# Kernel tuning notes

Hardware: AMD Instinct MI355X
Metric: run time of the kernel (lower is better)

## Reference

```python
import jax, jax.numpy as jnp
import numpy as np

N = 12000       # num nodes
E = 384000      # num edges (avg degree 32)
F_IN = 512      # num_feats
H = 64          # gnn_hid_dim (== anchor_dim)
C = 7           # num_cls
SIGMA = 1.0


def setup_inputs() -> dict:
    key = jax.random.key(0)
    ks = jax.random.split(key, 9)
    scale = lambda fan_in: 1.0 / np.sqrt(fan_in)
    return {
        "x": jax.random.normal(ks[0], (N, F_IN), dtype=jnp.float32),
        "W1": jax.random.normal(ks[1], (F_IN, H), dtype=jnp.float32) * scale(F_IN),
        "b1": jnp.zeros((H,), dtype=jnp.float32),
        "W2": jax.random.normal(ks[2], (H, H), dtype=jnp.float32) * scale(H),
        "b2": jnp.zeros((H,), dtype=jnp.float32),
        "aux": jax.random.normal(ks[3], (H,), dtype=jnp.float32),
        "clf_W": jax.random.normal(ks[4], (2 * H, C), dtype=jnp.float32) * scale(2 * H),
        "clf_b": jnp.zeros((C,), dtype=jnp.float32),
        "edge_index": jax.random.randint(ks[5], (2, E), 0, N, dtype=jnp.int64),
    }


def gcn_conv(x, W, b, src, dst, n):
    # GCNConv: D^{-1/2} (A + I) D^{-1/2} X W + b, with self-loops
    h = x @ W                                                   # [N, out]
    deg = jax.ops.segment_sum(jnp.ones(src.shape[0], h.dtype), dst,
                              num_segments=n) + 1.0             # +1 for self-loop
    inv_sqrt = jax.lax.rsqrt(deg)
    norm = inv_sqrt[src] * inv_sqrt[dst]                        # [E]
    agg = jax.ops.segment_sum(h[src] * norm[:, None], dst, num_segments=n)
    agg = agg + h / deg[:, None]                                # self-loop term (norm = 1/deg)
    return agg + b


def reference(x, W1, b1, W2, b2, aux, clf_W, clf_b, edge_index):
    src, dst = edge_index[0], edge_index[1]
    n = x.shape[0]
    h = jax.nn.relu(gcn_conv(x, W1, b1, src, dst, n))
    h = gcn_conv(h, W2, b2, src, dst, n)                        # [N, H]
    # kernel aggregate: pairwise Gaussian kernel on cosine scores
    a = aux / jnp.maximum(jnp.linalg.norm(aux), 1e-12)          # F.normalize
    hn = jnp.maximum(jnp.linalg.norm(h, axis=-1), 1e-8)         # cosine_similarity eps
    score = (h @ a) / hn                                        # [N]
    diff = score[None, :] - score[:, None]                      # [N, N]
    kappa = jnp.exp(-(diff * diff) / (SIGMA * SIGMA))           # [N, N]
    z = (kappa @ h) / jnp.sum(kappa, axis=1, keepdims=True)     # [N, H]
    return jnp.concatenate([h, z], axis=-1) @ clf_W + clf_b     # [N, C]
```

## Files before the change

### kernel.cpp

```cpp
#include <hip/hip_runtime.h>
#include <hip/hip_bf16.h>
#include <hip/hip_fp16.h>

#define N_NODES 12000
#define N_EDGES 384000
#define F_IN 512
#define H 64
#define C_CLS 7
#define KTERMS 16
#define PAD 96
#define CSTR 32
#define MOM_BLKS 768
#define MSTR 1040
#define NB 4
#define GEMM_BLKS 188
#define FILL_BLKS 324

typedef __attribute__((ext_vector_type(8))) short bf16x8;
typedef __attribute__((ext_vector_type(4))) float f32x4;

__device__ __forceinline__ float wred_f(float x) {
    #pragma unroll
    for (int o = 32; o > 0; o >>= 1) x += __shfl_xor(x, o);
    return x;
}

__global__ __launch_bounds__(256) void init_k(const float* __restrict__ W1,
                                              unsigned short* __restrict__ w1Th,
                                              unsigned short* __restrict__ w1Tl,
                                              int* __restrict__ cur,
                                              double* __restrict__ M8) {
    int i = blockIdx.x * 256 + threadIdx.x;
    if (i < 64 * 512) {
        int n = i >> 9, k = i & 511;
        float v = W1[k * 64 + n];
        unsigned xb = __float_as_uint(v);
        float hf = __uint_as_float(xb & 0xffff0000u);
        w1Th[i] = (unsigned short)(xb >> 16);
        w1Tl[i] = (unsigned short)(__float_as_uint(v - hf) >> 16);
    }
    if (i < N_NODES) cur[i * CSTR] = 0;
    if (i < 8 * MSTR) M8[i] = 0.0;
}

__global__ __launch_bounds__(256) void k1_gemm_fill(const float* __restrict__ x,
                                                    const unsigned short* __restrict__ w1Th,
                                                    const unsigned short* __restrict__ w1Tl,
                                                    const int* __restrict__ ei,
                                                    __half* __restrict__ hbufH,
                                                    int* __restrict__ cur,
                                                    int* __restrict__ csrc) {
    const int b = blockIdx.x, t = threadIdx.x;
    if (b < GEMM_BLKS) {
        __shared__ unsigned short wh[64 * 72];
        __shared__ unsigned short wl[64 * 72];
        const int l = t & 63, w = t >> 6;
        const int lm = l & 15, lk = l >> 4;
        const int i0 = b * 64;
        const int arow = min(i0 + w * 16 + lm, N_NODES - 1);
        const float* xrow = x + (size_t)arow * F_IN;
        f32x4 acc[4];
        #pragma unroll
        for (int c = 0; c < 4; ++c) acc[c] = (f32x4){0.f, 0.f, 0.f, 0.f};
        for (int kc = 0; kc < 8; ++kc) {
            #pragma unroll
            for (int q = 0; q < 2; ++q) {
                int idx = t + q * 256;
                int n = idx >> 3, kg = idx & 7;
                *(uint4*)(&wh[n * 72 + kg * 8]) =
                    *(const uint4*)(w1Th + n * 512 + kc * 64 + kg * 8);
                *(uint4*)(&wl[n * 72 + kg * 8]) =
                    *(const uint4*)(w1Tl + n * 512 + kc * 64 + kg * 8);
            }
            __syncthreads();
            #pragma unroll
            for (int ks = 0; ks < 2; ++ks) {
                float4 v0 = *(const float4*)(xrow + kc * 64 + ks * 32 + lk * 8);
                float4 v1 = *(const float4*)(xrow + kc * 64 + ks * 32 + lk * 8 + 4);
                float xv[8] = {v0.x, v0.y, v0.z, v0.w, v1.x, v1.y, v1.z, v1.w};
                bf16x8 ah, al;
                #pragma unroll
                for (int j = 0; j < 8; ++j) {
                    unsigned xb = __float_as_uint(xv[j]);
                    float hf = __uint_as_float(xb & 0xffff0000u);
                    ah[j] = (short)(xb >> 16);
                    al[j] = (short)(__float_as_uint(xv[j] - hf) >> 16);
                }
                #pragma unroll
                for (int c = 0; c < 4; ++c) {
                    bf16x8 bh = *(const bf16x8*)(&wh[(c * 16 + lm) * 72 + ks * 32 + lk * 8]);
                    bf16x8 bl = *(const bf16x8*)(&wl[(c * 16 + lm) * 72 + ks * 32 + lk * 8]);
                    acc[c] = __builtin_amdgcn_mfma_f32_16x16x32_bf16(ah, bh, acc[c], 0, 0, 0);
                    acc[c] = __builtin_amdgcn_mfma_f32_16x16x32_bf16(ah, bl, acc[c], 0, 0, 0);
                    acc[c] = __builtin_amdgcn_mfma_f32_16x16x32_bf16(al, bh, acc[c], 0, 0, 0);
                }
            }
            __syncthreads();
        }
        #pragma unroll
        for (int c = 0; c < 4; ++c) {
            #pragma unroll
            for (int r = 0; r < 4; ++r) {
                int row = i0 + w * 16 + lk * 4 + r;
                if (row < N_NODES)
                    hbufH[(size_t)row * H + c * 16 + lm] = __float2half(acc[c][r]);
            }
        }
    } else {
        for (int e = (b - GEMM_BLKS) * 256 + t; e < N_EDGES; e += FILL_BLKS * 256) {
            int s = ei[e];
            int d = ei[N_EDGES + e];
            int pos = atomicAdd(&cur[d * CSTR], 1);
            if (pos < PAD) csrc[d * PAD + pos] = s;
        }
    }
}

__global__ __launch_bounds__(256) void agg1_k(const __half* __restrict__ hbufH,
                                              const float* __restrict__ b1,
                                              const int* __restrict__ cur,
                                              const int* __restrict__ csrc,
                                              __half* __restrict__ h1H) {
    __shared__ int2 sPair[NB * PAD];
    __shared__ int sDeg[NB];
    __shared__ float sIsd[NB];
    const int t = threadIdx.x, f = t & 63, w = t >> 6;
    const int base = blockIdx.x * NB;
    if (t < NB) {
        int d = cur[(base + t) * CSTR];
        sDeg[t] = min(d, PAD);
        sIsd[t] = rsqrtf((float)d + 1.f);
    }
    __syncthreads();
    for (int idx = t; idx < NB * PAD; idx += 256) {
        int n = idx / PAD, e = idx - n * PAD;
        if (e < sDeg[n]) {
            int s = csrc[(base + n) * PAD + e];
            sPair[idx] = make_int2(s, __float_as_int(rsqrtf((float)cur[s * CSTR] + 1.f)));
        }
    }
    __syncthreads();
    const int i = base + w;
    const int deg = sDeg[w];
    const float isd = sIsd[w];
    const int2* pp = sPair + w * PAD;
    float acc = 0.f;
    int e = 0;
    for (; e + 16 <= deg; e += 16) {
        float part = 0.f;
        #pragma unroll
        for (int u = 0; u < 16; ++u) {
            int2 p = pp[e + u];
            part += __half2float(hbufH[p.x * H + f]) * __int_as_float(p.y);
        }
        acc += part;
    }
    for (; e + 4 <= deg; e += 4) {
        int2 p0 = pp[e], p1 = pp[e+1], p2 = pp[e+2], p3 = pp[e+3];
        acc += __half2float(hbufH[p0.x * H + f]) * __int_as_float(p0.y)
             + __half2float(hbufH[p1.x * H + f]) * __int_as_float(p1.y)
             + __half2float(hbufH[p2.x * H + f]) * __int_as_float(p2.y)
             + __half2float(hbufH[p3.x * H + f]) * __int_as_float(p3.y);
    }
    for (; e < deg; ++e) {
        int2 p = pp[e];
        acc += __half2float(hbufH[p.x * H + f]) * __int_as_float(p.y);
    }
    float res = (acc + __half2float(hbufH[i * H + f]) * isd) * isd + b1[f];
    h1H[i * H + f] = __float2half(fmaxf(res, 0.f));
}

__global__ __launch_bounds__(256) void agg2_k(const __half* __restrict__ h1H,
                                              const float* __restrict__ W2,
                                              const float* __restrict__ b2,
                                              const float* __restrict__ aux,
                                              const int* __restrict__ cur,
                                              const int* __restrict__ csrc,
                                              __half* __restrict__ h2H,
                                              float* __restrict__ score) {
    __shared__ float w2s[64 * 64];
    __shared__ int2 sPair[NB * PAD];
    __shared__ int sDeg[NB];
    __shared__ float sIsd[NB];
    __shared__ float anorm[64];
    __shared__ float gsh[NB * 64];
    const int t = threadIdx.x, f = t & 63, w = t >> 6;
    const int base = blockIdx.x * NB;
    #pragma unroll
    for (int q = 0; q < 4; ++q) {
        int idx = t + q * 256;
        int r = idx >> 4, c4 = idx & 15;
        *(float4*)(&w2s[r * 64 + c4 * 4]) = *(const float4*)(W2 + r * H + c4 * 4);
    }
    if (t < NB) {
        int d = cur[(base + t) * CSTR];
        sDeg[t] = min(d, PAD);
        sIsd[t] = rsqrtf((float)d + 1.f);
    }
    if (t < 64) {
        float av = aux[t];
        anorm[t] = av * rsqrtf(fmaxf(wred_f(av * av), 1e-24f));
    }
    __syncthreads();
    for (int idx = t; idx < NB * PAD; idx += 256) {
        int n = idx / PAD, e = idx - n * PAD;
        if (e < sDeg[n]) {
            int s = csrc[(base + n) * PAD + e];
            sPair[idx] = make_int2(s, __float_as_int(rsqrtf((float)cur[s * CSTR] + 1.f)));
        }
    }
    __syncthreads();
    const int i = base + w;
    const int deg = sDeg[w];
    const float isd = sIsd[w];
    const int2* pp = sPair + w * PAD;
    float acc = 0.f;
    int e = 0;
    for (; e + 16 <= deg; e += 16) {
        float part = 0.f;
        #pragma unroll
        for (int u = 0; u < 16; ++u) {
            int2 p = pp[e + u];
            part += __half2float(h1H[p.x * H + f]) * __int_as_float(p.y);
        }
        acc += part;
    }
    for (; e + 4 <= deg; e += 4) {
        int2 p0 = pp[e], p1 = pp[e+1], p2 = pp[e+2], p3 = pp[e+3];
        acc += __half2float(h1H[p0.x * H + f]) * __int_as_float(p0.y)
             + __half2float(h1H[p1.x * H + f]) * __int_as_float(p1.y)
             + __half2float(h1H[p2.x * H + f]) * __int_as_float(p2.y)
             + __half2float(h1H[p3.x * H + f]) * __int_as_float(p3.y);
    }
    for (; e < deg; ++e) {
        int2 p = pp[e];
        acc += __half2float(h1H[p.x * H + f]) * __int_as_float(p.y);
    }
    float g = (acc + __half2float(h1H[i * H + f]) * isd) * isd;
    gsh[w * 64 + f] = g;
    __builtin_amdgcn_wave_barrier();
    float hv = b2[f];
    #pragma unroll 16
    for (int k = 0; k < 64; ++k) hv += gsh[w * 64 + k] * w2s[k * 64 + f];
    h2H[i * H + f] = __float2half(hv);
    float dp = wred_f(hv * anorm[f]);
    float nn = wred_f(hv * hv);
    if (f == 0) score[i] = dp / fmaxf(sqrtf(nn), 1e-8f);
}

__global__ __launch_bounds__(256) void momden_k(const __half* __restrict__ h2H,
                                                const float* __restrict__ score,
                                                double* __restrict__ M8) {
    const int t = threadIdx.x, f = t & 63, g = t >> 6;
    float accM[KTERMS], accD[KTERMS];
    #pragma unroll
    for (int k = 0; k < KTERMS; ++k) { accM[k] = 0.f; accD[k] = 0.f; }
    for (int j = blockIdx.x * 4 + g; j < N_NODES; j += MOM_BLKS * 4) {
        float sj = score[j];
        float wj = expf(-sj * sj);
        float hv = __half2float(h2H[j * H + f]);
        float tm = wj * hv, td = wj;
        #pragma unroll
        for (int k = 0; k < KTERMS; ++k) {
            accM[k] += tm; tm *= sj;
            accD[k] += td; td *= sj;
        }
    }
    __shared__ float Msh[4 * KTERMS * 64];
    __shared__ float Dsh[4 * KTERMS];
    #pragma unroll
    for (int k = 0; k < KTERMS; ++k) Msh[(g * KTERMS + k) * 64 + f] = accM[k];
    if (f == 0) {
        #pragma unroll
        for (int k = 0; k < KTERMS; ++k) Dsh[g * KTERMS + k] = accD[k];
    }
    __syncthreads();
    double* Mc = M8 + (size_t)(blockIdx.x & 7) * MSTR;
    for (int idx = t; idx < KTERMS * 64; idx += 256) {
        int k = idx >> 6, ff = idx & 63;
        float sum = Msh[(0 * KTERMS + k) * 64 + ff] + Msh[(1 * KTERMS + k) * 64 + ff]
                  + Msh[(2 * KTERMS + k) * 64 + ff] + Msh[(3 * KTERMS + k) * 64 + ff];
        unsafeAtomicAdd(&Mc[idx], (double)sum);
    }
    if (t < KTERMS) {
        float sum = Dsh[t] + Dsh[KTERMS + t] + Dsh[2 * KTERMS + t] + Dsh[3 * KTERMS + t];
        unsafeAtomicAdd(&Mc[1024 + t], (double)sum);
    }
}

__global__ __launch_bounds__(256) void final_k(const __half* __restrict__ h2H,
                                               const float* __restrict__ score,
                                               const double* __restrict__ M8,
                                               const float* __restrict__ clfW,
                                               const float* __restrict__ clfb,
                                               float* __restrict__ out) {
    __shared__ float Ms[KTERMS * 64];
    __shared__ float m0s[KTERMS];
    __shared__ float cw[128 * C_CLS];
    __shared__ float cb[8];
    __shared__ float zh[4 * 128];
    const int t = threadIdx.x, f = t & 63, w = t >> 6;
    for (int idx = t; idx < KTERMS * 64; idx += 256) {
        double s = 0.0;
        #pragma unroll
        for (int c = 0; c < 8; ++c) s += M8[(size_t)c * MSTR + idx];
        Ms[idx] = (float)s;
    }
    if (t < KTERMS) {
        double s = 0.0;
        #pragma unroll
        for (int c = 0; c < 8; ++c) s += M8[(size_t)c * MSTR + 1024 + t];
        m0s[t] = (float)s;
    }
    for (int idx = t; idx < 128 * C_CLS; idx += 256) cw[idx] = clfW[idx];
    if (t < C_CLS) cb[t] = clfb[t];
    __syncthreads();
    const int base = blockIdx.x * 16;
    for (int q = 0; q < 4; ++q) {
        int i = base + q * 4 + w;
        float s = score[i];
        float c = expf(-s * s);
        float t2 = 2.f * s;
        float num = 0.f, den = 0.f;
        #pragma unroll
        for (int k = 0; k < KTERMS; ++k) {
            num += c * Ms[k * 64 + f];
            den += c * m0s[k];
            c *= t2 * (1.0f / (float)(k + 1));
        }
        zh[w * 128 + f] = __half2float(h2H[i * H + f]);
        zh[w * 128 + 64 + f] = num / den;
        __builtin_amdgcn_wave_barrier();
        if (f < C_CLS) {
            float o = cb[f];
            #pragma unroll 8
            for (int u = 0; u < 128; ++u) o += zh[w * 128 + u] * cw[u * C_CLS + f];
            out[(size_t)i * C_CLS + f] = o;
        }
        __builtin_amdgcn_wave_barrier();
    }
}

extern "C" void kernel_launch(void* const* d_in, const int* in_sizes, int n_in,
                              void* d_out, int out_size, void* d_ws, size_t ws_size,
                              hipStream_t stream) {
    (void)in_sizes; (void)n_in; (void)out_size; (void)ws_size;
    const float* x    = (const float*)d_in[0];
    const float* W1   = (const float*)d_in[1];
    const float* b1   = (const float*)d_in[2];
    const float* W2   = (const float*)d_in[3];
    const float* b2   = (const float*)d_in[4];
    const float* aux  = (const float*)d_in[5];
    const float* clfW = (const float*)d_in[6];
    const float* clfb = (const float*)d_in[7];
    const int*   ei   = (const int*)d_in[8];
    float* out = (float*)d_out;
    char* ws = (char*)d_ws;

    __half* hbufH = (__half*)(ws + 0);
    __half* h1H   = (__half*)(ws + 1536000);
    __half* h2H   = (__half*)(ws + 3072000);
    float*  score = (float*)(ws + 4608000);
    int*    csrc  = (int*)  (ws + 4656000);
    int*    cur   = (int*)  (ws + 9264000);
    double* M8    = (double*)(ws + 10800000);
    unsigned short* w1Th = (unsigned short*)(ws + 10866560);
    unsigned short* w1Tl = (unsigned short*)(ws + 10932096);

    init_k<<<128, 256, 0, stream>>>(W1, w1Th, w1Tl, cur, M8);
    k1_gemm_fill<<<GEMM_BLKS + FILL_BLKS, 256, 0, stream>>>(x, w1Th, w1Tl, ei,
                                                            hbufH, cur, csrc);
    agg1_k<<<N_NODES / NB, 256, 0, stream>>>(hbufH, b1, cur, csrc, h1H);
    agg2_k<<<N_NODES / NB, 256, 0, stream>>>(h1H, W2, b2, aux, cur, csrc, h2H, score);
    momden_k<<<MOM_BLKS, 256, 0, stream>>>(h2H, score, M8);
    final_k<<<750, 256, 0, stream>>>(h2H, score, M8, clfW, clfb, out);
}
```

Measured before the change: 87.24 us.

## Double-buffer W1 tiles in GEMM and reuse edge pairs across aggregation kernels

The first-layer GEMM now double-buffers the W1 hi/lo tiles in shared memory and prefetches the next x chunk into registers, so global loads overlap the MFMA work and one barrier per iteration is removed. agg1 also writes its (source, normalization) pairs to a workspace buffer. agg2 then copies these pairs with vector loads instead of re-gathering csrc and the scattered degree counts. This costs double the LDS in the GEMM blocks and an extra global write in agg1. The agg2 copy reads full padded slots, some of which hold garbage past each node's degree, but those entries are never used.

Measured after the change: 89.30 us. 1.02x slower.

```diff
diff --git a/kernel.cpp b/kernel.cpp
--- a/kernel.cpp
+++ b/kernel.cpp
@@ -52,8 +52,8 @@
                                                     int* __restrict__ csrc) {
     const int b = blockIdx.x, t = threadIdx.x;
     if (b < GEMM_BLKS) {
-        __shared__ unsigned short wh[64 * 72];
-        __shared__ unsigned short wl[64 * 72];
+        __shared__ unsigned short wh[2][64 * 72];
+        __shared__ unsigned short wl[2][64 * 72];
         const int l = t & 63, w = t >> 6;
         const int lm = l & 15, lk = l >> 4;
         const int i0 = b * 64;
@@ -62,22 +62,47 @@
         f32x4 acc[4];
         #pragma unroll
         for (int c = 0; c < 4; ++c) acc[c] = (f32x4){0.f, 0.f, 0.f, 0.f};
+
+        #define STAGE_W(KC, BUF)                                                   \
+            do {                                                                   \
+                _Pragma("unroll")                                                  \
+                for (int q = 0; q < 2; ++q) {                                      \
+                    int idx = t + q * 256;                                         \
+                    int n = idx >> 3, kg = idx & 7;                                \
+                    *(uint4*)(&wh[BUF][n * 72 + kg * 8]) =                         \
+                        *(const uint4*)(w1Th + n * 512 + (KC) * 64 + kg * 8);      \
+                    *(uint4*)(&wl[BUF][n * 72 + kg * 8]) =                         \
+                        *(const uint4*)(w1Tl + n * 512 + (KC) * 64 + kg * 8);      \
+                }                                                                  \
+            } while (0)
+
+        float4 a0 = *(const float4*)(xrow + lk * 8);
+        float4 a1 = *(const float4*)(xrow + lk * 8 + 4);
+        float4 g0 = *(const float4*)(xrow + 32 + lk * 8);
+        float4 g1 = *(const float4*)(xrow + 32 + lk * 8 + 4);
+        STAGE_W(0, 0);
+        __syncthreads();
         for (int kc = 0; kc < 8; ++kc) {
-            #pragma unroll
-            for (int q = 0; q < 2; ++q) {
-                int idx = t + q * 256;
-                int n = idx >> 3, kg = idx & 7;
-                *(uint4*)(&wh[n * 72 + kg * 8]) =
-                    *(const uint4*)(w1Th + n * 512 + kc * 64 + kg * 8);
-                *(uint4*)(&wl[n * 72 + kg * 8]) =
-                    *(const uint4*)(w1Tl + n * 512 + kc * 64 + kg * 8);
+            const int cb = kc & 1;
+            float4 ca0 = a0, ca1 = a1, cg0 = g0, cg1 = g1;
+            if (kc < 7) {
+                const float* nx = xrow + (kc + 1) * 64;
+                a0 = *(const float4*)(nx + lk * 8);
+                a1 = *(const float4*)(nx + lk * 8 + 4);
+                g0 = *(const float4*)(nx + 32 + lk * 8);
+                g1 = *(const float4*)(nx + 32 + lk * 8 + 4);
+                STAGE_W(kc + 1, cb ^ 1);
             }
-            __syncthreads();
             #pragma unroll
             for (int ks = 0; ks < 2; ++ks) {
-                float4 v0 = *(const float4*)(xrow + kc * 64 + ks * 32 + lk * 8);
-                float4 v1 = *(const float4*)(xrow + kc * 64 + ks * 32 + lk * 8 + 4);
-                float xv[8] = {v0.x, v0.y, v0.z, v0.w, v1.x, v1.y, v1.z, v1.w};
+                float xv[8];
+                if (ks == 0) {
+                    xv[0]=ca0.x; xv[1]=ca0.y; xv[2]=ca0.z; xv[3]=ca0.w;
+                    xv[4]=ca1.x; xv[5]=ca1.y; xv[6]=ca1.z; xv[7]=ca1.w;
+                } else {
+                    xv[0]=cg0.x; xv[1]=cg0.y; xv[2]=cg0.z; xv[3]=cg0.w;
+                    xv[4]=cg1.x; xv[5]=cg1.y; xv[6]=cg1.z; xv[7]=cg1.w;
+                }
                 bf16x8 ah, al;
                 #pragma unroll
                 for (int j = 0; j < 8; ++j) {
@@ -88,8 +113,8 @@
                 }
                 #pragma unroll
                 for (int c = 0; c < 4; ++c) {
-                    bf16x8 bh = *(const bf16x8*)(&wh[(c * 16 + lm) * 72 + ks * 32 + lk * 8]);
-                    bf16x8 bl = *(const bf16x8*)(&wl[(c * 16 + lm) * 72 + ks * 32 + lk * 8]);
+                    bf16x8 bh = *(const bf16x8*)(&wh[cb][(c * 16 + lm) * 72 + ks * 32 + lk * 8]);
+                    bf16x8 bl = *(const bf16x8*)(&wl[cb][(c * 16 + lm) * 72 + ks * 32 + lk * 8]);
                     acc[c] = __builtin_amdgcn_mfma_f32_16x16x32_bf16(ah, bh, acc[c], 0, 0, 0);
                     acc[c] = __builtin_amdgcn_mfma_f32_16x16x32_bf16(ah, bl, acc[c], 0, 0, 0);
                     acc[c] = __builtin_amdgcn_mfma_f32_16x16x32_bf16(al, bh, acc[c], 0, 0, 0);
@@ -97,6 +122,7 @@
             }
             __syncthreads();
         }
+        #undef STAGE_W
         #pragma unroll
         for (int c = 0; c < 4; ++c) {
             #pragma unroll
@@ -120,7 +146,8 @@
                                               const float* __restrict__ b1,
                                               const int* __restrict__ cur,
                                               const int* __restrict__ csrc,
-                                              __half* __restrict__ h1H) {
+                                              __half* __restrict__ h1H,
+                                              int2* __restrict__ pairs) {
     __shared__ int2 sPair[NB * PAD];
     __shared__ int sDeg[NB];
     __shared__ float sIsd[NB];
@@ -136,7 +163,9 @@
         int n = idx / PAD, e = idx - n * PAD;
         if (e < sDeg[n]) {
             int s = csrc[(base + n) * PAD + e];
-            sPair[idx] = make_int2(s, __float_as_int(rsqrtf((float)cur[s * CSTR] + 1.f)));
+            int2 v = make_int2(s, __float_as_int(rsqrtf((float)cur[s * CSTR] + 1.f)));
+            sPair[idx] = v;
+            pairs[base * PAD + idx] = v;
         }
     }
     __syncthreads();
@@ -175,7 +204,7 @@
                                               const float* __restrict__ b2,
                                               const float* __restrict__ aux,
                                               const int* __restrict__ cur,
-                                              const int* __restrict__ csrc,
+                                              const int2* __restrict__ pairs,
                                               __half* __restrict__ h2H,
                                               float* __restrict__ score) {
     __shared__ float w2s[64 * 64];
@@ -201,13 +230,10 @@
         float av = aux[t];
         anorm[t] = av * rsqrtf(fmaxf(wred_f(av * av), 1e-24f));
     }
-    __syncthreads();
-    for (int idx = t; idx < NB * PAD; idx += 256) {
-        int n = idx / PAD, e = idx - n * PAD;
-        if (e < sDeg[n]) {
-            int s = csrc[(base + n) * PAD + e];
-            sPair[idx] = make_int2(s, __float_as_int(rsqrtf((float)cur[s * CSTR] + 1.f)));
-        }
+    {
+        const int4* src = (const int4*)(pairs + base * PAD);
+        int4* dst = (int4*)sPair;
+        if (t < NB * PAD / 2) dst[t] = src[t];
     }
     __syncthreads();
     const int i = base + w;
@@ -366,12 +392,13 @@
     double* M8    = (double*)(ws + 10800000);
     unsigned short* w1Th = (unsigned short*)(ws + 10866560);
     unsigned short* w1Tl = (unsigned short*)(ws + 10932096);
+    int2*   pairs = (int2*)(ws + 10997632);
 
     init_k<<<128, 256, 0, stream>>>(W1, w1Th, w1Tl, cur, M8);
     k1_gemm_fill<<<GEMM_BLKS + FILL_BLKS, 256, 0, stream>>>(x, w1Th, w1Tl, ei,
                                                             hbufH, cur, csrc);
-    agg1_k<<<N_NODES / NB, 256, 0, stream>>>(hbufH, b1, cur, csrc, h1H);
-    agg2_k<<<N_NODES / NB, 256, 0, stream>>>(h1H, W2, b2, aux, cur, csrc, h2H, score);
+    agg1_k<<<N_NODES / NB, 256, 0, stream>>>(hbufH, b1, cur, csrc, h1H, pairs);
+    agg2_k<<<N_NODES / NB, 256, 0, stream>>>(h1H, W2, b2, aux, cur, pairs, h2H, score);
     momden_k<<<MOM_BLKS, 256, 0, stream>>>(h2H, score, M8);
     final_k<<<750, 256, 0, stream>>>(h2H, score, M8, clfW, clfb, out);
 }
```
